# Optimization experiments

Measured on AMD Instinct MI355X. Metric: run time of the kernel, lower is better.

Reference implementation:

```python
import jax, jax.numpy as jnp
import numpy as np

N_NODES = 100000
N_EDGES = 1600000
D_IN = 128
D_HID = 128
D_OUT = 10
N_GRAPHS = 512


def _sage_conv(x, src, dst, W_l, b_l, W_r, num_nodes):
    # PyG SAGEConv (mean aggr): out = lin_l(mean_{j in N(i)} x_j) + lin_r(x_i)
    msg = x[src]                                            # [E, D] gather
    s = jax.ops.segment_sum(msg, dst, num_segments=num_nodes)
    cnt = jax.ops.segment_sum(jnp.ones((src.shape[0], 1), x.dtype), dst,
                              num_segments=num_nodes)
    mean = s / jnp.maximum(cnt, 1.0)                        # 0 where no neighbors
    return mean @ W_l.T + b_l + x @ W_r.T


def setup_inputs() -> dict:
    key = jax.random.key(0)
    ks = jax.random.split(key, 10)
    glorot = lambda k, o, i: jax.random.normal(k, (o, i), jnp.float32) * (1.0 / np.sqrt(i))
    return {
        "x": jax.random.normal(ks[0], (N_NODES, D_IN), jnp.float32),
        "edge_index": jax.random.randint(ks[1], (2, N_EDGES), 0, N_NODES, jnp.int64),
        "batch": jnp.sort(jax.random.randint(ks[2], (N_NODES,), 0, N_GRAPHS, jnp.int64)),
        "W1_l": glorot(ks[3], D_HID, D_IN),
        "b1": jnp.zeros((D_HID,), jnp.float32),
        "W1_r": glorot(ks[4], D_HID, D_IN),
        "W2_l": glorot(ks[5], D_HID, D_HID),
        "b2": jnp.zeros((D_HID,), jnp.float32),
        "W2_r": glorot(ks[6], D_HID, D_HID),
        "Wf": glorot(ks[7], D_OUT, D_HID),
        "bf": jnp.zeros((D_OUT,), jnp.float32),
    }


def reference(x, edge_index, batch, W1_l, b1, W1_r, W2_l, b2, W2_r, Wf, bf):
    src, dst = edge_index[0], edge_index[1]
    n = x.shape[0]
    h = jax.nn.relu(_sage_conv(x, src, dst, W1_l, b1, W1_r, n))
    h = jax.nn.relu(_sage_conv(h, src, dst, W2_l, b2, W2_r, n))
    # global_mean_pool over graph ids
    gsum = jax.ops.segment_sum(h, batch, num_segments=N_GRAPHS)
    gcnt = jax.ops.segment_sum(jnp.ones((n, 1), h.dtype), batch, num_segments=N_GRAPHS)
    g = gsum / jnp.maximum(gcnt, 1.0)
    logits = g @ Wf.T + bf
    return jax.nn.log_softmax(logits, axis=-1)
```

## Files before the change

### kernel.cpp

```cpp
#include <hip/hip_runtime.h>
#include <hip/hip_bf16.h>

#define N_NODES 100000
#define N_EDGES 1600000
#define N_GRAPHS 512
#define NB 256
#define NPB 391
#define CHUNK 6250
#define STAGE 7680
#define GGROUPS 1563
#define GGRID 512

typedef __attribute__((ext_vector_type(8))) short short8;
typedef __attribute__((ext_vector_type(4))) float f32x4;
typedef __attribute__((ext_vector_type(2))) float f32x2;

__device__ __forceinline__ float b2f(ushort u) {
    union { unsigned int i; float f; } c; c.i = ((unsigned int)u) << 16; return c.f;
}
__device__ __forceinline__ float blo(unsigned int u) {
    union { unsigned int i; float f; } c; c.i = u << 16; return c.f;
}
__device__ __forceinline__ float bhi(unsigned int u) {
    union { unsigned int i; float f; } c; c.i = u & 0xffff0000u; return c.f;
}
__device__ __forceinline__ ushort f2b(float f) {
    union { float f; unsigned int i; } c; c.f = f;
    unsigned int r = (c.i + 0x7fffu + ((c.i >> 16) & 1u)) >> 16;
    return (ushort)r;
}
__device__ __forceinline__ unsigned int fbits(float f) {
    union { float f; unsigned int i; } c; c.f = f; return c.i;
}
__device__ __forceinline__ int idx_at(const void* p, long i, int f) {
    return f ? (int)((const long long*)p)[i] : ((const int*)p)[i];
}
__device__ __forceinline__ short8 dec8(const uchar* p) {
    uint2 q = *(const uint2*)p;
    f32x2 d0 = __builtin_amdgcn_cvt_pk_f32_fp8((int)q.x, false);
    f32x2 d1 = __builtin_amdgcn_cvt_pk_f32_fp8((int)q.x, true);
    f32x2 d2 = __builtin_amdgcn_cvt_pk_f32_fp8((int)q.y, false);
    f32x2 d3 = __builtin_amdgcn_cvt_pk_f32_fp8((int)q.y, true);
    union { short8 s; unsigned int u[4]; } r;
    r.u[0] = __builtin_amdgcn_perm(fbits(d0.y), fbits(d0.x), 0x07060302u);
    r.u[1] = __builtin_amdgcn_perm(fbits(d1.y), fbits(d1.x), 0x07060302u);
    r.u[2] = __builtin_amdgcn_perm(fbits(d2.y), fbits(d2.x), 0x07060302u);
    r.u[3] = __builtin_amdgcn_perm(fbits(d3.y), fbits(d3.x), 0x07060302u);
    return r.s;
}

__global__ __launch_bounds__(256) void k_prep(const void* __restrict__ ei,
                                              const void* __restrict__ x,
                                              unsigned int* __restrict__ xf8,
                                              const void* W1l, const void* W1r,
                                              const void* W2l, const void* W2r,
                                              const void* b1,  const void* b2,
                                              ushort* __restrict__ wbf,
                                              int* __restrict__ blkcnt,
                                              float* __restrict__ gsum,
                                              int* __restrict__ flags) {
    int b = blockIdx.x, t = threadIdx.x;
    __shared__ int cf, ce, cb;
    int f0 = 0, f1 = 0, f2 = 0;
    if (b < NB + 2048 + 257) {
        if (t == 0) { cf = 0; ce = 0; cb = 0; }
        __syncthreads();
        unsigned int w = ((const unsigned int*)x)[t];
        unsigned int e = (w >> 7) & 0xffu;
        if (e >= 110u && e <= 130u) atomicAdd(&cf, 1);
        if (t < 128) {
            if (((const unsigned int*)ei)[2 * t + 1] != 0u) atomicAdd(&ce, 1);
            if (((const int*)x == nullptr) ? 0 : 0) {}
        }
        __syncthreads();
        f0 = (cf >= 128) ? 1 : 0;
        f1 = (ce == 0) ? 1 : 0;
        (void)f2;
    }
    if (b == 0) {
        __shared__ int cbb;
        if (t == 0) cbb = 0;
        __syncthreads();
    }
    if (b < NB) {
        __shared__ int h[NB];
        for (int j = t; j < NB; j += 256) h[j] = 0;
        __syncthreads();
        int lo = b * CHUNK, hi = lo + CHUNK;
        for (int e = lo + t; e < hi; e += 256) {
            int d = idx_at(ei, (long)N_EDGES + e, f1);
            atomicAdd(&h[d / NPB], 1);
        }
        __syncthreads();
        if (t < NB) blkcnt[b * NB + t] = h[t];
    } else if (b < NB + 2048) {
        bool f32src = (f0 == 0);
        int vb = b - NB;
        const long nG = (long)N_NODES * 128 / 4;
        for (long g = (long)vb * 256 + t; g < nG; g += 2048L * 256) {
            float v0, v1, v2, v3;
            if (f32src) {
                float4 vv = ((const float4*)x)[g];
                v0 = vv.x; v1 = vv.y; v2 = vv.z; v3 = vv.w;
            } else {
                uint2 q = ((const uint2*)x)[g];
                v0 = blo(q.x); v1 = bhi(q.x); v2 = blo(q.y); v3 = bhi(q.y);
            }
            int r = __builtin_amdgcn_cvt_pk_fp8_f32(v0, v1, 0, false);
            r = __builtin_amdgcn_cvt_pk_fp8_f32(v2, v3, r, true);
            xf8[g] = (unsigned int)r;
        }
    } else if (b < NB + 2048 + 257) {
        int idx = (b - NB - 2048) * 256 + t;
        if (idx >= 65792) return;
        const void* src; int off;
        if      (idx < 16384) { src = W1l; off = idx; }
        else if (idx < 32768) { src = W1r; off = idx - 16384; }
        else if (idx < 49152) { src = W2l; off = idx - 32768; }
        else if (idx < 65536) { src = W2r; off = idx - 49152; }
        else if (idx < 65664) { src = b1;  off = idx - 65536; }
        else                  { src = b2;  off = idx - 65664; }
        wbf[idx] = (f0 != 0) ? ((const ushort*)src)[off]
                             : f2b(((const float*)src)[off]);
    } else {
        int idx = (b - NB - 2048 - 257) * 256 + t;
        gsum[idx] = 0.f;
    }
    (void)flags;
}

__global__ __launch_bounds__(256) void k_flags(const unsigned int* __restrict__ xw,
                                               const unsigned int* __restrict__ ew,
                                               const int* __restrict__ bw,
                                               int* __restrict__ flags) {
    __shared__ int cf, ce, cb;
    int t = threadIdx.x;
    if (t == 0) { cf = 0; ce = 0; cb = 0; }
    __syncthreads();
    unsigned int w = xw[t];
    unsigned int e = (w >> 7) & 0xffu;
    if (e >= 110u && e <= 130u) atomicAdd(&cf, 1);
    if (t < 128) {
        if (ew[2 * t + 1] != 0u) atomicAdd(&ce, 1);
        if (bw[99001 + 2 * t] != 0) atomicAdd(&cb, 1);
    }
    __syncthreads();
    if (t == 0) {
        flags[0] = (cf >= 128) ? 1 : 0;
        flags[1] = (ce == 0) ? 1 : 0;
        flags[2] = (cb == 0) ? 1 : 0;
    }
}

__global__ __launch_bounds__(NB) void k_bscan(const int* __restrict__ blkcnt,
                                              int* __restrict__ bucketBase,
                                              int* __restrict__ blkbase) {
    __shared__ int s[NB];
    int t = threadIdx.x;
    int tot = 0;
    for (int blk = 0; blk < NB; ++blk) tot += blkcnt[blk * NB + t];
    s[t] = tot; __syncthreads();
    for (int off = 1; off < NB; off <<= 1) {
        int a = (t >= off) ? s[t - off] : 0;
        __syncthreads();
        s[t] += a;
        __syncthreads();
    }
    int excl = s[t] - tot;
    bucketBase[t] = excl;
    if (t == NB - 1) bucketBase[NB] = s[NB - 1];
    int run = excl;
    for (int blk = 0; blk < NB; ++blk) {
        blkbase[blk * NB + t] = run;
        run += blkcnt[blk * NB + t];
    }
}

__global__ __launch_bounds__(256) void k_bin(const void* __restrict__ ei,
                                             const int* __restrict__ blkbase,
                                             int* __restrict__ binned,
                                             const int* __restrict__ flags) {
    __shared__ int bb[NB];
    __shared__ int rank[NB];
    int t = threadIdx.x, blk = blockIdx.x;
    int f = flags[1];
    for (int j = t; j < NB; j += 256) { bb[j] = blkbase[blk * NB + j]; rank[j] = 0; }
    __syncthreads();
    int lo = blk * CHUNK, hi = lo + CHUNK;
    for (int e = lo + t; e < hi; e += 256) {
        int s = idx_at(ei, e, f);
        int d = idx_at(ei, (long)N_EDGES + e, f);
        int b = d / NPB;
        int loc = d - b * NPB;
        int r = atomicAdd(&rank[b], 1);
        binned[bb[b] + r] = s | (loc << 20);
    }
}

__global__ __launch_bounds__(256) void k_csr(const int* __restrict__ binned,
                                             const int* __restrict__ bucketBase,
                                             int* __restrict__ rowptr,
                                             int* __restrict__ csr) {
    __shared__ int cnt[400];
    __shared__ int sc[400];
    __shared__ int sh[256];
    __shared__ int stage[STAGE];
    int t = threadIdx.x, b = blockIdx.x;
    int nodeLo = b * NPB;
    int nC = N_NODES - nodeLo; if (nC > NPB) nC = NPB;
    int eBase = bucketBase[b], eEnd = bucketBase[b + 1];

    for (int j = t; j < 400; j += 256) cnt[j] = 0;
    __syncthreads();
    for (int i = eBase + t; i < eEnd; i += 256)
        atomicAdd(&cnt[binned[i] >> 20], 1);
    __syncthreads();
    int base = t * 2;
    int v0 = (base < 400) ? cnt[base] : 0;
    int v1 = (base + 1 < 400) ? cnt[base + 1] : 0;
    int ssum = v0 + v1;
    sh[t] = ssum; __syncthreads();
    for (int off = 1; off < 256; off <<= 1) {
        int a = (t >= off) ? sh[t - off] : 0;
        __syncthreads();
        sh[t] += a;
        __syncthreads();
    }
    int pre = sh[t] - ssum;
    if (base < 400) sc[base] = pre;
    if (base + 1 < 400) sc[base + 1] = pre + v0;
    __syncthreads();
    for (int j = t; j < nC; j += 256) rowptr[nodeLo + j] = eBase + sc[j];
    if (b == NB - 1) {
        if (t == 0) rowptr[N_NODES] = eEnd;
        if (t < 64) csr[N_EDGES + t] = 0;
    }
    for (int j = t; j < 400; j += 256) cnt[j] = 0;
    __syncthreads();
    for (int i = eBase + t; i < eEnd; i += 256) {
        int p = binned[i];
        int loc = p >> 20;
        int pos = sc[loc] + atomicAdd(&cnt[loc], 1);
        int srcn = p & 0xFFFFF;
        if (pos < STAGE) stage[pos] = srcn;
        else csr[eBase + pos] = srcn;
    }
    __syncthreads();
    int eCnt = eEnd - eBase; if (eCnt > STAGE) eCnt = STAGE;
    for (int j = t; j < eCnt; j += 256) csr[eBase + j] = stage[j];
}

__global__ __launch_bounds__(256) void k_agg(const uint4* __restrict__ x8,
                                             const int* __restrict__ rowptr,
                                             const int* __restrict__ csr,
                                             uint4* __restrict__ mout) {
    int wv = blockIdx.x * 4 + (threadIdx.x >> 6);
    int lane = threadIdx.x & 63;
    int li = lane & 7;
    int node = wv * 8 + (lane >> 3);
    int beg = rowptr[node];
    int end = rowptr[node + 1];
    int deg = end - beg;
    f32x2 a2[8] = {};
    int full16 = deg & ~15;
    int full8 = deg & ~7;
    int j = 0;
    for (; j < full16; j += 16) {
        int vidx0 = csr[beg + j + li];
        int vidx1 = csr[beg + j + 8 + li];
        uint4 p[8], p2[8];
#pragma unroll
        for (int i = 0; i < 8; ++i) {
            int idx = __shfl(vidx0, i | (lane & 56));
            p[i] = x8[(long)idx * 8 + li];
        }
#pragma unroll
        for (int i = 0; i < 8; ++i) {
            int idx = __shfl(vidx1, i | (lane & 56));
            p2[i] = x8[(long)idx * 8 + li];
        }
#pragma unroll
        for (int i = 0; i < 8; ++i) {
            a2[0] += __builtin_amdgcn_cvt_pk_f32_fp8((int)p[i].x, false);
            a2[1] += __builtin_amdgcn_cvt_pk_f32_fp8((int)p[i].x, true);
            a2[2] += __builtin_amdgcn_cvt_pk_f32_fp8((int)p[i].y, false);
            a2[3] += __builtin_amdgcn_cvt_pk_f32_fp8((int)p[i].y, true);
            a2[4] += __builtin_amdgcn_cvt_pk_f32_fp8((int)p[i].z, false);
            a2[5] += __builtin_amdgcn_cvt_pk_f32_fp8((int)p[i].z, true);
            a2[6] += __builtin_amdgcn_cvt_pk_f32_fp8((int)p[i].w, false);
            a2[7] += __builtin_amdgcn_cvt_pk_f32_fp8((int)p[i].w, true);
        }
#pragma unroll
        for (int i = 0; i < 8; ++i) {
            a2[0] += __builtin_amdgcn_cvt_pk_f32_fp8((int)p2[i].x, false);
            a2[1] += __builtin_amdgcn_cvt_pk_f32_fp8((int)p2[i].x, true);
            a2[2] += __builtin_amdgcn_cvt_pk_f32_fp8((int)p2[i].y, false);
            a2[3] += __builtin_amdgcn_cvt_pk_f32_fp8((int)p2[i].y, true);
            a2[4] += __builtin_amdgcn_cvt_pk_f32_fp8((int)p2[i].z, false);
            a2[5] += __builtin_amdgcn_cvt_pk_f32_fp8((int)p2[i].z, true);
            a2[6] += __builtin_amdgcn_cvt_pk_f32_fp8((int)p2[i].w, false);
            a2[7] += __builtin_amdgcn_cvt_pk_f32_fp8((int)p2[i].w, true);
        }
    }
    for (; j < full8; j += 8) {
        int vidx = csr[beg + j + li];
        uint4 p[8];
#pragma unroll
        for (int i = 0; i < 8; ++i) {
            int idx = __shfl(vidx, i | (lane & 56));
            p[i] = x8[(long)idx * 8 + li];
        }
#pragma unroll
        for (int i = 0; i < 8; ++i) {
            a2[0] += __builtin_amdgcn_cvt_pk_f32_fp8((int)p[i].x, false);
            a2[1] += __builtin_amdgcn_cvt_pk_f32_fp8((int)p[i].x, true);
            a2[2] += __builtin_amdgcn_cvt_pk_f32_fp8((int)p[i].y, false);
            a2[3] += __builtin_amdgcn_cvt_pk_f32_fp8((int)p[i].y, true);
            a2[4] += __builtin_amdgcn_cvt_pk_f32_fp8((int)p[i].z, false);
            a2[5] += __builtin_amdgcn_cvt_pk_f32_fp8((int)p[i].z, true);
            a2[6] += __builtin_amdgcn_cvt_pk_f32_fp8((int)p[i].w, false);
            a2[7] += __builtin_amdgcn_cvt_pk_f32_fp8((int)p[i].w, true);
        }
    }
    if (j < deg) {
        int pos = beg + j + li;
        if (pos > end - 1) pos = end - 1;
        int vidx = csr[pos];
#pragma unroll
        for (int i = 0; i < 8; ++i) {
            int idx = __shfl(vidx, i | (lane & 56));
            uint4 p = x8[(long)idx * 8 + li];
            bool ok = (j + i < deg);
            unsigned int q0 = ok ? p.x : 0u;
            unsigned int q1 = ok ? p.y : 0u;
            unsigned int q2 = ok ? p.z : 0u;
            unsigned int q3 = ok ? p.w : 0u;
            a2[0] += __builtin_amdgcn_cvt_pk_f32_fp8((int)q0, false);
            a2[1] += __builtin_amdgcn_cvt_pk_f32_fp8((int)q0, true);
            a2[2] += __builtin_amdgcn_cvt_pk_f32_fp8((int)q1, false);
            a2[3] += __builtin_amdgcn_cvt_pk_f32_fp8((int)q1, true);
            a2[4] += __builtin_amdgcn_cvt_pk_f32_fp8((int)q2, false);
            a2[5] += __builtin_amdgcn_cvt_pk_f32_fp8((int)q2, true);
            a2[6] += __builtin_amdgcn_cvt_pk_f32_fp8((int)q3, false);
            a2[7] += __builtin_amdgcn_cvt_pk_f32_fp8((int)q3, true);
        }
    }
    float s = (deg > 0) ? 1.f / (float)deg : 0.f;
    uint4 o;
    int r;
    r = __builtin_amdgcn_cvt_pk_fp8_f32(a2[0].x * s, a2[0].y * s, 0, false);
    r = __builtin_amdgcn_cvt_pk_fp8_f32(a2[1].x * s, a2[1].y * s, r, true);  o.x = (unsigned int)r;
    r = __builtin_amdgcn_cvt_pk_fp8_f32(a2[2].x * s, a2[2].y * s, 0, false);
    r = __builtin_amdgcn_cvt_pk_fp8_f32(a2[3].x * s, a2[3].y * s, r, true);  o.y = (unsigned int)r;
    r = __builtin_amdgcn_cvt_pk_fp8_f32(a2[4].x * s, a2[4].y * s, 0, false);
    r = __builtin_amdgcn_cvt_pk_fp8_f32(a2[5].x * s, a2[5].y * s, r, true);  o.z = (unsigned int)r;
    r = __builtin_amdgcn_cvt_pk_fp8_f32(a2[6].x * s, a2[6].y * s, 0, false);
    r = __builtin_amdgcn_cvt_pk_fp8_f32(a2[7].x * s, a2[7].y * s, r, true);  o.w = (unsigned int)r;
    mout[(long)node * 8 + li] = o;
}

__global__ __launch_bounds__(512, 2) void k_gemm(const uchar* __restrict__ A0f8,
                                                 const uchar* __restrict__ A1f8,
                                                 const ushort* __restrict__ Wl,
                                                 const ushort* __restrict__ Wr,
                                                 const ushort* __restrict__ bias,
                                                 uchar* __restrict__ out8,
                                                 float* __restrict__ gsum,
                                                 const void* __restrict__ batch,
                                                 const int* __restrict__ flags,
                                                 int layer1) {
    __shared__ short Ws[4096 * 8];
    int t = threadIdx.x;
#pragma unroll
    for (int i = 0; i < 8; ++i) {
        int f = i * 512 + t;
        int ln = f & 63, kk = (f >> 6) & 7, tile = f >> 9;
        int o = tile * 16 + (ln & 15);
        int k0 = kk * 32 + ((ln >> 4) * 8);
        const ushort* wsrc = (k0 < 128) ? (Wl + o * 128 + k0)
                                        : (Wr + o * 128 + (k0 - 128));
        *(short8*)&Ws[f * 8] = *(const short8*)wsrc;
    }
    __syncthreads();

    int half = t >> 8;
    int tt = t & 255;
    int wid = tt >> 6, lane = tt & 63;
    int kq = (lane >> 4) * 8;
    int bflag = layer1 ? 0 : flags[2];

    float bo8[8];
#pragma unroll
    for (int tile = 0; tile < 8; ++tile)
        bo8[tile] = b2f(bias[tile * 16 + (lane & 15)]);

    int h = blockIdx.x * 2 + half;
    int gbeg = (h * GGROUPS) >> 10;
    int gend = ((h + 1) * GGROUPS) >> 10;

    for (int g = gbeg; g < gend; ++g) {
        long nbase = (long)g * 64 + (long)wid * 16;
        int arow = (int)nbase + (lane & 15);
        if (arow >= N_NODES) arow = N_NODES - 1;

        short8 afrag[8];
#pragma unroll
        for (int kk = 0; kk < 8; ++kk) {
            int k0 = kk * 32 + kq;
            afrag[kk] = (k0 < 128)
                ? dec8(A0f8 + (long)arow * 128 + k0)
                : dec8(A1f8 + (long)arow * 128 + (k0 - 128));
        }

        int bg[4]; int guni = 0; bool uniform = false;
        if (!layer1) {
            int bmin = 0x7fffffff, bmax = -0x7fffffff;
#pragma unroll
            for (int r = 0; r < 4; ++r) {
                long node = nbase + (lane >> 4) * 4 + r;
                if (node < N_NODES) {
                    int bb = idx_at(batch, node, bflag);
                    bg[r] = bb;
                    bmin = min(bmin, bb); bmax = max(bmax, bb);
                } else { bg[r] = 0; bmax = 0x7fffffff; }
            }
            bmin = min(bmin, __shfl_xor(bmin, 16));
            bmin = min(bmin, __shfl_xor(bmin, 32));
            bmax = max(bmax, __shfl_xor(bmax, 16));
            bmax = max(bmax, __shfl_xor(bmax, 32));
            uniform = (bmin == bmax);
            guni = bmin;
        }

#pragma unroll 1
        for (int tile = 0; tile < 8; ++tile) {
            f32x4 acc = {0.f, 0.f, 0.f, 0.f};
#pragma unroll
            for (int kk = 0; kk < 8; ++kk) {
                short8 bfrag = *(short8*)&Ws[((tile * 8 + kk) * 64 + lane) * 8];
                acc = __builtin_amdgcn_mfma_f32_16x16x32_bf16(afrag[kk], bfrag, acc, 0, 0, 0);
            }
            int o = tile * 16 + (lane & 15);
            float bo = bo8[tile];
            if (layer1) {
#pragma unroll
                for (int r = 0; r < 4; ++r) {
                    long node = nbase + (lane >> 4) * 4 + r;
                    if (node < N_NODES) {
                        float v = acc[r] + bo;
                        v = v > 0.f ? v : 0.f;
                        int pp = __builtin_amdgcn_cvt_pk_fp8_f32(v, v, 0, false);
                        out8[node * 128 + o] = (uchar)pp;
                    }
                }
            } else if (uniform) {
                float s = 0.f;
#pragma unroll
                for (int r = 0; r < 4; ++r) {
                    float v = acc[r] + bo;
                    s += (v > 0.f ? v : 0.f);
                }
                s += __shfl_xor(s, 16);
                s += __shfl_xor(s, 32);
                if ((lane >> 4) == 0) atomicAdd(&gsum[guni * 128 + o], s);
            } else {
#pragma unroll
                for (int r = 0; r < 4; ++r) {
                    long node = nbase + (lane >> 4) * 4 + r;
                    if (node < N_NODES) {
                        float v = acc[r] + bo;
                        v = v > 0.f ? v : 0.f;
                        atomicAdd(&gsum[bg[r] * 128 + o], v);
                    }
                }
            }
        }
    }
}

__global__ __launch_bounds__(128) void k_cls(const float* __restrict__ gsum,
                                             const void* __restrict__ batch,
                                             const void* __restrict__ Wf,
                                             const void* __restrict__ bfv,
                                             void* __restrict__ outp,
                                             const int* __restrict__ flags) {
    int g = blockIdx.x, t = threadIdx.x;
    bool f32 = (flags[0] == 0);
    int b64 = flags[2];
    __shared__ int rng[2];
    __shared__ float gv[128];
    __shared__ float lg[10];
    if (t < 2) {
        int v = g + t, lo = 0, hi = N_NODES;
        while (lo < hi) {
            int mid = (lo + hi) >> 1;
            if (idx_at(batch, mid, b64) < v) lo = mid + 1; else hi = mid;
        }
        rng[t] = lo;
    }
    __syncthreads();
    int cnt = rng[1] - rng[0];
    float c = (cnt > 0) ? (float)cnt : 1.f;
    gv[t] = gsum[g * 128 + t] / c;
    __syncthreads();
    if (t < 10) {
        float s = f32 ? ((const float*)bfv)[t] : b2f(((const ushort*)bfv)[t]);
        for (int k = 0; k < 128; ++k) {
            float wv = f32 ? ((const float*)Wf)[t * 128 + k] : b2f(((const ushort*)Wf)[t * 128 + k]);
            s += gv[k] * wv;
        }
        lg[t] = s;
    }
    __syncthreads();
    if (t == 0) {
        float mx = lg[0];
        for (int i = 1; i < 10; ++i) mx = fmaxf(mx, lg[i]);
        float se = 0.f;
        for (int i = 0; i < 10; ++i) se += expf(lg[i] - mx);
        float lse = mx + logf(se);
        for (int i = 0; i < 10; ++i) {
            float v = lg[i] - lse;
            if (f32) ((float*)outp)[g * 10 + i] = v;
            else     ((ushort*)outp)[g * 10 + i] = f2b(v);
        }
    }
}

extern "C" void kernel_launch(void* const* d_in, const int* in_sizes, int n_in,
                              void* d_out, int out_size, void* d_ws, size_t ws_size,
                              hipStream_t stream) {
    const void* x     = d_in[0];
    const void* ei    = d_in[1];
    const void* batch = d_in[2];
    const void* W1l = d_in[3];
    const void* b1  = d_in[4];
    const void* W1r = d_in[5];
    const void* W2l = d_in[6];
    const void* b2  = d_in[7];
    const void* W2r = d_in[8];
    const void* Wf  = d_in[9];
    const void* bf_ = d_in[10];

    char* w = (char*)d_ws;
    int* flags      = (int*)(w + 0);
    int* rowptr     = (int*)(w + 640);
    ushort* wbf     = (ushort*)(w + 400768);
    int* csr        = (int*)(w + 532480);
    float* gsum     = (float*)(w + 6933248);
    uchar* mbuf     = (uchar*)(w + 32533248);
    int* bucketBase = (int*)(w + 32533248);
    int* blkcnt     = (int*)(w + 32534528);
    int* blkbase    = (int*)(w + 32796672);
    uchar* h1f8     = (uchar*)(w + 58133248);
    int* binned     = (int*)(w + 58133248);
    unsigned int* xf8 = (unsigned int*)(w + 70933248);

    dim3 blk256(256), blkNB(NB), blk128(128), blk512(512);

    k_flags<<<1, blk256, 0, stream>>>((const unsigned int*)x, (const unsigned int*)ei,
                                      (const int*)batch, flags);
    k_prep<<<NB + 2048 + 257 + 256, blk256, 0, stream>>>(ei, x, xf8,
                                                         W1l, W1r, W2l, W2r, b1, b2,
                                                         wbf, blkcnt, gsum, flags);
    k_bscan<<<1, blkNB, 0, stream>>>(blkcnt, bucketBase, blkbase);
    k_bin<<<NB, blk256, 0, stream>>>(ei, blkbase, binned, flags);
    k_csr<<<NB, blk256, 0, stream>>>(binned, bucketBase, rowptr, csr);

    int agrid = N_NODES / 8 / 4;

    k_agg<<<agrid, blk256, 0, stream>>>((const uint4*)xf8, rowptr, csr, (uint4*)mbuf);
    k_gemm<<<GGRID, blk512, 0, stream>>>(mbuf, (const uchar*)xf8,
                                         wbf + 0, wbf + 16384, wbf + 65536,
                                         h1f8, (float*)nullptr, nullptr, flags, 1);
    k_agg<<<agrid, blk256, 0, stream>>>((const uint4*)h1f8, rowptr, csr, (uint4*)mbuf);
    k_gemm<<<GGRID, blk512, 0, stream>>>(mbuf, h1f8,
                                         wbf + 32768, wbf + 49152, wbf + 65664,
                                         (uchar*)nullptr, gsum, batch, flags, 0);
    k_cls<<<N_GRAPHS, blk128, 0, stream>>>(gsum, batch, Wf, bf_, d_out, flags);
}
```

Before: 286.8 us.

## Parallelize bucket prefix scan across blocks with transposed block counts

The single-block bucket scan walked all 256 source blocks serially per bucket. It is now split in two: 256 blocks each scan one bucket's counts across source blocks (blkcnt is stored transposed), then one small block scans the per-bucket totals. k_bin adds the bucket base to the per-block offset itself. This adds one extra kernel launch in exchange for removing a long serial loop on a single block.

```diff
diff --git a/kernel.cpp b/kernel.cpp
--- a/kernel.cpp
+++ b/kernel.cpp
@@ -49,6 +49,29 @@
     return r.s;
 }
 
+__global__ __launch_bounds__(256) void k_flags(const unsigned int* __restrict__ xw,
+                                               const unsigned int* __restrict__ ew,
+                                               const int* __restrict__ bw,
+                                               int* __restrict__ flags) {
+    __shared__ int cf, ce, cb;
+    int t = threadIdx.x;
+    if (t == 0) { cf = 0; ce = 0; cb = 0; }
+    __syncthreads();
+    unsigned int w = xw[t];
+    unsigned int e = (w >> 7) & 0xffu;
+    if (e >= 110u && e <= 130u) atomicAdd(&cf, 1);
+    if (t < 128) {
+        if (ew[2 * t + 1] != 0u) atomicAdd(&ce, 1);
+        if (bw[99001 + 2 * t] != 0) atomicAdd(&cb, 1);
+    }
+    __syncthreads();
+    if (t == 0) {
+        flags[0] = (cf >= 128) ? 1 : 0;
+        flags[1] = (ce == 0) ? 1 : 0;
+        flags[2] = (cb == 0) ? 1 : 0;
+    }
+}
+
 __global__ __launch_bounds__(256) void k_prep(const void* __restrict__ ei,
                                               const void* __restrict__ x,
                                               unsigned int* __restrict__ xf8,
@@ -57,30 +80,22 @@
                                               const void* b1,  const void* b2,
                                               ushort* __restrict__ wbf,
                                               int* __restrict__ blkcnt,
-                                              float* __restrict__ gsum,
-                                              int* __restrict__ flags) {
+                                              float* __restrict__ gsum) {
     int b = blockIdx.x, t = threadIdx.x;
-    __shared__ int cf, ce, cb;
-    int f0 = 0, f1 = 0, f2 = 0;
+    __shared__ int cf, ce;
+    int f0 = 0, f1 = 0;
     if (b < NB + 2048 + 257) {
-        if (t == 0) { cf = 0; ce = 0; cb = 0; }
+        if (t == 0) { cf = 0; ce = 0; }
         __syncthreads();
         unsigned int w = ((const unsigned int*)x)[t];
         unsigned int e = (w >> 7) & 0xffu;
         if (e >= 110u && e <= 130u) atomicAdd(&cf, 1);
         if (t < 128) {
             if (((const unsigned int*)ei)[2 * t + 1] != 0u) atomicAdd(&ce, 1);
-            if (((const int*)x == nullptr) ? 0 : 0) {}
         }
         __syncthreads();
         f0 = (cf >= 128) ? 1 : 0;
         f1 = (ce == 0) ? 1 : 0;
-        (void)f2;
-    }
-    if (b == 0) {
-        __shared__ int cbb;
-        if (t == 0) cbb = 0;
-        __syncthreads();
     }
     if (b < NB) {
         __shared__ int h[NB];
@@ -92,7 +107,7 @@
             atomicAdd(&h[d / NPB], 1);
         }
         __syncthreads();
-        if (t < NB) blkcnt[b * NB + t] = h[t];
+        if (t < NB) blkcnt[t * NB + b] = h[t];
     } else if (b < NB + 2048) {
         bool f32src = (f0 == 0);
         int vb = b - NB;
@@ -126,65 +141,54 @@
         int idx = (b - NB - 2048 - 257) * 256 + t;
         gsum[idx] = 0.f;
     }
-    (void)flags;
-}
-
-__global__ __launch_bounds__(256) void k_flags(const unsigned int* __restrict__ xw,
-                                               const unsigned int* __restrict__ ew,
-                                               const int* __restrict__ bw,
-                                               int* __restrict__ flags) {
-    __shared__ int cf, ce, cb;
-    int t = threadIdx.x;
-    if (t == 0) { cf = 0; ce = 0; cb = 0; }
-    __syncthreads();
-    unsigned int w = xw[t];
-    unsigned int e = (w >> 7) & 0xffu;
-    if (e >= 110u && e <= 130u) atomicAdd(&cf, 1);
-    if (t < 128) {
-        if (ew[2 * t + 1] != 0u) atomicAdd(&ce, 1);
-        if (bw[99001 + 2 * t] != 0) atomicAdd(&cb, 1);
-    }
-    __syncthreads();
-    if (t == 0) {
-        flags[0] = (cf >= 128) ? 1 : 0;
-        flags[1] = (ce == 0) ? 1 : 0;
-        flags[2] = (cb == 0) ? 1 : 0;
-    }
-}
-
-__global__ __launch_bounds__(NB) void k_bscan(const int* __restrict__ blkcnt,
-                                              int* __restrict__ bucketBase,
-                                              int* __restrict__ blkbase) {
+}
+
+__global__ __launch_bounds__(NB) void k_bscan_a(const int* __restrict__ blkcnt,
+                                                int* __restrict__ blkbase,
+                                                int* __restrict__ tot) {
+    __shared__ int s[NB];
+    int j = blockIdx.x, t = threadIdx.x;
+    int v = blkcnt[j * NB + t];
+    s[t] = v; __syncthreads();
+    for (int off = 1; off < NB; off <<= 1) {
+        int a = (t >= off) ? s[t - off] : 0;
+        __syncthreads();
+        s[t] += a;
+        __syncthreads();
+    }
+    blkbase[j * NB + t] = s[t] - v;
+    if (t == NB - 1) tot[j] = s[t];
+}
+
+__global__ __launch_bounds__(NB) void k_bscan_b(const int* __restrict__ tot,
+                                                int* __restrict__ bucketBase) {
     __shared__ int s[NB];
     int t = threadIdx.x;
-    int tot = 0;
-    for (int blk = 0; blk < NB; ++blk) tot += blkcnt[blk * NB + t];
-    s[t] = tot; __syncthreads();
+    int v = tot[t];
+    s[t] = v; __syncthreads();
     for (int off = 1; off < NB; off <<= 1) {
         int a = (t >= off) ? s[t - off] : 0;
         __syncthreads();
         s[t] += a;
         __syncthreads();
     }
-    int excl = s[t] - tot;
-    bucketBase[t] = excl;
-    if (t == NB - 1) bucketBase[NB] = s[NB - 1];
-    int run = excl;
-    for (int blk = 0; blk < NB; ++blk) {
-        blkbase[blk * NB + t] = run;
-        run += blkcnt[blk * NB + t];
-    }
+    bucketBase[t] = s[t] - v;
+    if (t == NB - 1) bucketBase[NB] = s[t];
 }
 
 __global__ __launch_bounds__(256) void k_bin(const void* __restrict__ ei,
                                              const int* __restrict__ blkbase,
+                                             const int* __restrict__ bucketBase,
                                              int* __restrict__ binned,
                                              const int* __restrict__ flags) {
     __shared__ int bb[NB];
     __shared__ int rank[NB];
     int t = threadIdx.x, blk = blockIdx.x;
     int f = flags[1];
-    for (int j = t; j < NB; j += 256) { bb[j] = blkbase[blk * NB + j]; rank[j] = 0; }
+    for (int j = t; j < NB; j += 256) {
+        bb[j] = blkbase[j * NB + blk] + bucketBase[j];
+        rank[j] = 0;
+    }
     __syncthreads();
     int lo = blk * CHUNK, hi = lo + CHUNK;
     for (int e = lo + t; e < hi; e += 256) {
@@ -551,6 +555,7 @@
     int* bucketBase = (int*)(w + 32533248);
     int* blkcnt     = (int*)(w + 32534528);
     int* blkbase    = (int*)(w + 32796672);
+    int* tot        = (int*)(w + 33058816);
     uchar* h1f8     = (uchar*)(w + 58133248);
     int* binned     = (int*)(w + 58133248);
     unsigned int* xf8 = (unsigned int*)(w + 70933248);
@@ -561,9 +566,10 @@
                                       (const int*)batch, flags);
     k_prep<<<NB + 2048 + 257 + 256, blk256, 0, stream>>>(ei, x, xf8,
                                                          W1l, W1r, W2l, W2r, b1, b2,
-                                                         wbf, blkcnt, gsum, flags);
-    k_bscan<<<1, blkNB, 0, stream>>>(blkcnt, bucketBase, blkbase);
-    k_bin<<<NB, blk256, 0, stream>>>(ei, blkbase, binned, flags);
+                                                         wbf, blkcnt, gsum);
+    k_bscan_a<<<NB, blkNB, 0, stream>>>(blkcnt, blkbase, tot);
+    k_bscan_b<<<1, blkNB, 0, stream>>>(tot, bucketBase);
+    k_bin<<<NB, blk256, 0, stream>>>(ei, blkbase, bucketBase, binned, flags);
     k_csr<<<NB, blk256, 0, stream>>>(binned, bucketBase, rowptr, csr);
 
     int agrid = N_NODES / 8 / 4;
```

After: 279.5 us. -2.5%, faster.
